# Optimization experiments

Measured on AMD Instinct MI355X. Metric: run time of the kernel, lower is better.

The kernel has to match this reference:

```python
import jax, jax.numpy as jnp
import numpy as np

B, L, F = 256, 1800, 50
E, K, H, D = 4, 2, 32, 64
MAXH, HU = 900, 32


def setup_inputs() -> dict:
    key = jax.random.key(0)
    ks = jax.random.split(key, 24)
    s = 0.1
    nrm = lambda k, shape: jax.random.normal(k, shape, jnp.float32) * s
    return {
        "x": jax.random.normal(ks[0], (B, L, F), jnp.float32),
        "horizon": jax.random.randint(ks[1], (B,), 0, MAXH + 1),
        "W_in": nrm(ks[2], (D, F)), "b_in": nrm(ks[3], (D,)),
        "emb": nrm(ks[4], (MAXH + 1, D)),
        "W_gate": nrm(ks[5], (E, D)), "b_gate": nrm(ks[6], (E,)),
        "Wih0": nrm(ks[7], (E, 3 * H, D)), "Whh0": nrm(ks[8], (E, 3 * H, H)),
        "bih0": nrm(ks[9], (E, 3 * H)), "bhh0": nrm(ks[10], (E, 3 * H)),
        "Wih1": nrm(ks[11], (E, 3 * H, H)), "Whh1": nrm(ks[12], (E, 3 * H, H)),
        "bih1": nrm(ks[13], (E, 3 * H)), "bhh1": nrm(ks[14], (E, 3 * H)),
        "Wh1": nrm(ks[15], (E, HU, H)), "bh1": nrm(ks[16], (E, HU)),
        "Wh2": nrm(ks[17], (E, 1, HU)), "bh2": nrm(ks[18], (E, 1)),
    }


def _gru_layer(x_seq, Wih, Whh, bih, bhh):
    # x_seq: (L, B, Din). PyTorch GRU cell math (gate order r, z, n).
    xg = jnp.einsum('lbd,gd->lbg', x_seq, Wih) + bih  # (L, B, 3H)
    h0 = jnp.zeros((x_seq.shape[1], H), x_seq.dtype)

    def step(h, xgt):
        gh = h @ Whh.T + bhh
        r = jax.nn.sigmoid(xgt[:, :H] + gh[:, :H])
        z = jax.nn.sigmoid(xgt[:, H:2 * H] + gh[:, H:2 * H])
        n = jnp.tanh(xgt[:, 2 * H:] + r * gh[:, 2 * H:])
        h_new = (1.0 - z) * n + z * h
        return h_new, h_new

    h_last, hs = jax.lax.scan(step, h0, xg)
    return h_last, hs


def _expert(x_seq, Wih0, Whh0, bih0, bhh0, Wih1, Whh1, bih1, bhh1, Wh1, bh1, Wh2, bh2):
    _, hs0 = _gru_layer(x_seq, Wih0, Whh0, bih0, bhh0)      # layer 0: full sequence
    h1, _ = _gru_layer(hs0, Wih1, Whh1, bih1, bhh1)          # layer 1: final hidden (B, H)
    hid = jax.nn.relu(h1 @ Wh1.T + bh1)                      # head MLP (eval: dropout = id)
    return (hid @ Wh2.T + bh2)[:, 0]                         # (B,)


def reference(x, horizon, W_in, b_in, emb, W_gate, b_gate,
              Wih0, Whh0, bih0, bhh0, Wih1, Whh1, bih1, bhh1,
              Wh1, bh1, Wh2, bh2):
    x_proj = jnp.einsum('blf,df->bld', x, W_in) + b_in       # input_proj
    h_embed = emb[horizon]                                   # (B, D)
    x_proj = x_proj + h_embed[:, None, :]
    gate_logits = h_embed @ W_gate.T + b_gate                # (B, E)
    topk_logits, topk_idx = jax.lax.top_k(gate_logits, K)
    topk_w = jax.nn.softmax(topk_logits, axis=-1)
    Bn = x.shape[0]
    # dense routing weights (B, E): zero for non-routed experts -> identical math
    w_dense = jnp.zeros((Bn, E), x.dtype).at[jnp.arange(Bn)[:, None], topk_idx].add(topk_w)
    x_seq = jnp.transpose(x_proj, (1, 0, 2))                 # (L, B, D)
    preds = jax.vmap(_expert, in_axes=(None,) + (0,) * 12)(
        x_seq, Wih0, Whh0, bih0, bhh0, Wih1, Whh1, bih1, bhh1, Wh1, bh1, Wh2, bh2)  # (E, B)
    return jnp.sum(w_dense.T * preds, axis=0)                # (B,)
```

## Files before the change

kernel.cpp:

```cpp
#include <hip/hip_runtime.h>
#include <math.h>

#define NB   256
#define LSEQ 1800
#define NF   50
#define NE   4
#define NH   32
#define G3   96
#define ND   64
#define NHU  32
#define CHUNK 72
#define TBLK  8
#define NCHUNK (LSEQ / CHUNK)
#define NBLK   (CHUNK / TBLK)

typedef float v2f __attribute__((ext_vector_type(2)));

__device__ __forceinline__ v2f v2fma(v2f a, v2f b, v2f c) {
    return __builtin_elementwise_fma(a, b, c);
}
__device__ __forceinline__ v2f mkv2(float a, float b) { v2f t; t.x = a; t.y = b; return t; }
__device__ __forceinline__ v2f splat2(float s) { v2f t; t.x = s; t.y = s; return t; }

__global__ void compute_C_kernel(const float* __restrict__ Wih0,
                                 const float* __restrict__ W_in,
                                 float* __restrict__ Cg) {
    int e = blockIdx.x;
    for (int idx = threadIdx.x; idx < NF * G3; idx += blockDim.x) {
        int f = idx / G3;
        int g = idx - f * G3;
        const float* wr = Wih0 + ((size_t)e * G3 + g) * ND;
        float s = 0.f;
        #pragma unroll 8
        for (int d = 0; d < ND; d++) s += wr[d] * W_in[d * NF + f];
        Cg[(size_t)e * NF * G3 + idx] = s;
    }
}

__device__ __forceinline__ float fsig(float x) {
    float e = __builtin_amdgcn_exp2f(-1.442695041f * x);
    return __builtin_amdgcn_rcpf(1.f + e);
}
__device__ __forceinline__ float ftanh(float x) {
    x = fmaxf(x, -20.f);
    float e = __builtin_amdgcn_exp2f(-2.885390082f * x);
    return (1.f - e) * __builtin_amdgcn_rcpf(1.f + e);
}

__global__ __launch_bounds__(64, 1)
void moe_gru_kernel(const float* __restrict__ x,
                    const int*   __restrict__ horizon,
                    const float* __restrict__ emb,
                    const float* __restrict__ W_gate,
                    const float* __restrict__ b_gate,
                    const float* __restrict__ b_in,
                    const float* __restrict__ Wih0,
                    const float* __restrict__ Whh0,
                    const float* __restrict__ bih0,
                    const float* __restrict__ bhh0,
                    const float* __restrict__ Wih1,
                    const float* __restrict__ Whh1,
                    const float* __restrict__ bih1,
                    const float* __restrict__ bhh1,
                    const float* __restrict__ Wh1,
                    const float* __restrict__ bh1,
                    const float* __restrict__ Wh2,
                    const float* __restrict__ bh2,
                    const float* __restrict__ Cg,
                    float* __restrict__ out) {
    __shared__ __align__(16) float smem[4800 + 3600 + 64 + 64 + 32];
    float* CT  = smem;
    float* xs  = smem + 4800;
    float* heL = smem + 4800 + 3600;
    float* bbL = heL + 64;
    float* h1L = bbL + 64;

    const int bid = blockIdx.x;
    const int b   = bid >> 2;
    const int e   = bid & 3;
    const int tid = threadIdx.x;
    const int j   = tid & 31;
    const int hlf = tid >> 5;
    const int k0h = hlf << 4;

    {
        int hor = horizon[b];
        float he = emb[(size_t)hor * ND + tid];
        heL[tid] = he;
        bbL[tid] = he + b_in[tid];
    }

    float lg[NE];
    #pragma unroll
    for (int q = 0; q < NE; q++) {
        float s = b_gate[q];
        for (int d = 0; d < ND; d++) s += heL[d] * W_gate[q * ND + d];
        lg[q] = s;
    }
    int i1 = 0;
    #pragma unroll
    for (int q = 1; q < NE; q++) if (lg[q] > lg[i1]) i1 = q;
    int i2 = (i1 == 0) ? 1 : 0;
    #pragma unroll
    for (int q = 0; q < NE; q++) if (q != i1 && lg[q] > lg[i2]) i2 = q;
    if (e != i1 && e != i2) return;
    const float ex2 = expf(lg[i2] - lg[i1]);
    const float wgt = (e == i1) ? (1.f / (1.f + ex2)) : (ex2 / (1.f + ex2));

    for (int idx = tid; idx < NF * G3; idx += 64)
        CT[idx] = Cg[(size_t)e * NF * G3 + idx];

    v2f sA0[16], sA1[16], sA2[16];
    v2f wB0[8], wB1[8], wB2[8];
    {
        const float* baseA = (hlf ? Wih1 : Whh0) + (size_t)e * G3 * NH;
        const float* rA0 = baseA + (size_t)j * NH;
        const float* rA1 = baseA + (size_t)(j + 32) * NH;
        const float* rA2 = baseA + (size_t)(j + 64) * NH;
        #pragma unroll
        for (int q4 = 0; q4 < 8; q4++) {
            float4 qa = ((const float4*)rA0)[q4];
            sA0[2*q4] = mkv2(qa.x, qa.y); sA0[2*q4+1] = mkv2(qa.z, qa.w);
            float4 qb = ((const float4*)rA1)[q4];
            sA1[2*q4] = mkv2(qb.x, qb.y); sA1[2*q4+1] = mkv2(qb.z, qb.w);
            float4 qc = ((const float4*)rA2)[q4];
            sA2[2*q4] = mkv2(qc.x, qc.y); sA2[2*q4+1] = mkv2(qc.z, qc.w);
        }
        const float* baseB = Whh1 + (size_t)e * G3 * NH;
        const float* rB0 = baseB + (size_t)j * NH + k0h;
        const float* rB1 = baseB + (size_t)(j + 32) * NH + k0h;
        const float* rB2 = baseB + (size_t)(j + 64) * NH + k0h;
        #pragma unroll
        for (int q4 = 0; q4 < 4; q4++) {
            float4 qa = ((const float4*)rB0)[q4];
            wB0[2*q4] = mkv2(qa.x, qa.y); wB0[2*q4+1] = mkv2(qa.z, qa.w);
            float4 qb = ((const float4*)rB1)[q4];
            wB1[2*q4] = mkv2(qb.x, qb.y); wB1[2*q4+1] = mkv2(qb.z, qb.w);
            float4 qc = ((const float4*)rB2)[q4];
            wB2[2*q4] = mkv2(qc.x, qc.y); wB2[2*q4+1] = mkv2(qc.z, qc.w);
        }
    }
    const float selb0 = hlf ? bih1[e*G3 + j]      : bhh0[e*G3 + j];
    const float selb1 = hlf ? bih1[e*G3 + j + 32] : bhh0[e*G3 + j + 32];
    const float selb2 = hlf ? bih1[e*G3 + j + 64] : bhh0[e*G3 + j + 64];
    const float whb0  = hlf ? 0.f : bhh1[e*G3 + j];
    const float whb1  = hlf ? 0.f : bhh1[e*G3 + j + 32];
    const float whb2  = hlf ? 0.f : bhh1[e*G3 + j + 64];

    float dreg0, dreg1, dreg2;
    {
        float s0 = bih0[e*G3 + j], s1 = bih0[e*G3 + j + 32], s2 = bih0[e*G3 + j + 64];
        const float* w0 = Wih0 + ((size_t)e * G3 + j) * ND;
        const float* w1 = Wih0 + ((size_t)e * G3 + j + 32) * ND;
        const float* w2 = Wih0 + ((size_t)e * G3 + j + 64) * ND;
        for (int d = 0; d < ND; d++) {
            float bb = bbL[d];
            s0 += w0[d] * bb; s1 += w1[d] * bb; s2 += w2[d] * bb;
        }
        dreg0 = hlf ? 0.f : s0;
        dreg1 = hlf ? 0.f : s1;
        dreg2 = hlf ? 0.f : s2;
    }

    v2f h0v[16], h1v[8];
    #pragma unroll
    for (int k = 0; k < 16; k++) h0v[k] = splat2(0.f);
    #pragma unroll
    for (int k = 0; k < 8; k++)  h1v[k] = splat2(0.f);
    float hold = 0.f;
    float lmul = hlf ? 0.f : 1.f;
    if (tid < 32) h1L[tid] = 0.f;

    const float* xg = x + (size_t)b * LSEQ * NF;

    for (int ch = 0; ch < NCHUNK; ch++) {
        {
            const float4* xc4 = (const float4*)(xg + (size_t)ch * CHUNK * NF);
            for (int i4 = tid; i4 < (CHUNK * NF) / 4; i4 += 64) {
                float4 v = xc4[i4];
                int idx = i4 * 4;
                #pragma unroll
                for (int u = 0; u < 4; u++) {
                    int id = idx + u;
                    int it = (int)(((unsigned)id * 5243u) >> 18);
                    int f  = id - it * 50;
                    float val = (u == 0) ? v.x : (u == 1) ? v.y : (u == 2) ? v.z : v.w;
                    xs[f * CHUNK + it] = val;
                }
            }
        }

        for (int blk = 0; blk < NBLK; blk++) {
            const int ib0 = blk * TBLK;
            v2f a0[4], a1[4], a2[4];
            #pragma unroll
            for (int p = 0; p < 4; p++) {
                a0[p] = splat2(dreg0); a1[p] = splat2(dreg1); a2[p] = splat2(dreg2);
            }
            {
                const int fb = 25 * hlf;
                #pragma unroll 5
                for (int f = 0; f < 25; f++) {
                    const int fg = fb + f;
                    float c0 = CT[fg * G3 + j];
                    float c1 = CT[fg * G3 + j + 32];
                    float c2 = CT[fg * G3 + j + 64];
                    const float4* xp = (const float4*)(xs + fg * CHUNK + ib0);
                    float4 xa = xp[0], xb = xp[1];
                    v2f xv[4] = { mkv2(xa.x, xa.y), mkv2(xa.z, xa.w),
                                  mkv2(xb.x, xb.y), mkv2(xb.z, xb.w) };
                    v2f w0 = splat2(c0), w1 = splat2(c1), w2 = splat2(c2);
                    #pragma unroll
                    for (int p = 0; p < 4; p++) {
                        a0[p] = v2fma(w0, xv[p], a0[p]);
                        a1[p] = v2fma(w1, xv[p], a1[p]);
                        a2[p] = v2fma(w2, xv[p], a2[p]);
                    }
                }
            }
            #pragma unroll
            for (int p = 0; p < 4; p++) {
                a0[p].x += __shfl_xor(a0[p].x, 32, 64); a0[p].y += __shfl_xor(a0[p].y, 32, 64);
                a1[p].x += __shfl_xor(a1[p].x, 32, 64); a1[p].y += __shfl_xor(a1[p].y, 32, 64);
                a2[p].x += __shfl_xor(a2[p].x, 32, 64); a2[p].y += __shfl_xor(a2[p].y, 32, 64);
            }

            #pragma unroll
            for (int i = 0; i < TBLK; i++) {
                v2f dB0 = mkv2(whb0, 0.f), dB1 = mkv2(whb1, 0.f), dB2 = mkv2(whb2, 0.f);
                #pragma unroll
                for (int k = 0; k < 8; k++) {
                    dB0 = v2fma(wB0[k], h1v[k], dB0);
                    dB1 = v2fma(wB1[k], h1v[k], dB1);
                    dB2 = v2fma(wB2[k], h1v[k], dB2);
                }
                float B0 = dB0.x + dB0.y, B1 = dB1.x + dB1.y, B2 = dB2.x + dB2.y;
                float R0 = B0 + __shfl_xor(B0, 32, 64);
                float R1 = B1 + __shfl_xor(B1, 32, 64);
                float R2 = B2 + __shfl_xor(B2, 32, 64);
                v2f dA0 = mkv2(selb0, 0.f), dA1 = mkv2(selb1, 0.f), dA2 = mkv2(selb2, 0.f);
                #pragma unroll
                for (int k = 0; k < 16; k++) {
                    dA0 = v2fma(sA0[k], h0v[k], dA0);
                    dA1 = v2fma(sA1[k], h0v[k], dA1);
                    dA2 = v2fma(sA2[k], h0v[k], dA2);
                }
                float A0 = dA0.x + dA0.y, A1 = dA1.x + dA1.y, A2 = dA2.x + dA2.y;
                const float ac0 = a0[i >> 1][i & 1];
                const float ac1 = a1[i >> 1][i & 1];
                const float ac2 = a2[i >> 1][i & 1];
                float o0   = hlf ? R0 : ac0;
                float o1   = hlf ? R1 : ac1;
                float npre = hlf ? A2 : ac2;
                float gn   = hlf ? R2 : A2;
                float r = fsig(A0 + o0);
                float z = fsig(A1 + o1);
                float n = ftanh(npre + r * gn);
                float hnew = (n + z * (hold - n)) * lmul;
                hold = hnew;
                lmul = 1.f;
                if (hlf) h1L[j] = hnew;
                const float4* h1q = (const float4*)(h1L + k0h);
                float4 q0 = h1q[0], q1 = h1q[1], q2 = h1q[2], q3 = h1q[3];
                h1v[0] = mkv2(q0.x, q0.y); h1v[1] = mkv2(q0.z, q0.w);
                h1v[2] = mkv2(q1.x, q1.y); h1v[3] = mkv2(q1.z, q1.w);
                h1v[4] = mkv2(q2.x, q2.y); h1v[5] = mkv2(q2.z, q2.w);
                h1v[6] = mkv2(q3.x, q3.y); h1v[7] = mkv2(q3.z, q3.w);
                {
                    int hni = __float_as_int(hnew);
                    #pragma unroll
                    for (int k = 0; k < 16; k++) {
                        float e0 = __int_as_float(__builtin_amdgcn_readlane(hni, 2*k));
                        float e1 = __int_as_float(__builtin_amdgcn_readlane(hni, 2*k+1));
                        h0v[k] = mkv2(e0, e1);
                    }
                }
            }
        }
    }

    {
        v2f dA0 = mkv2(selb0, 0.f), dA1 = mkv2(selb1, 0.f), dA2 = mkv2(selb2, 0.f);
        #pragma unroll
        for (int k = 0; k < 16; k++) {
            dA0 = v2fma(sA0[k], h0v[k], dA0);
            dA1 = v2fma(sA1[k], h0v[k], dA1);
            dA2 = v2fma(sA2[k], h0v[k], dA2);
        }
        v2f dB0 = mkv2(whb0, 0.f), dB1 = mkv2(whb1, 0.f), dB2 = mkv2(whb2, 0.f);
        #pragma unroll
        for (int k = 0; k < 8; k++) {
            dB0 = v2fma(wB0[k], h1v[k], dB0);
            dB1 = v2fma(wB1[k], h1v[k], dB1);
            dB2 = v2fma(wB2[k], h1v[k], dB2);
        }
        float A0 = dA0.x + dA0.y, A1 = dA1.x + dA1.y, A2 = dA2.x + dA2.y;
        float B0 = dB0.x + dB0.y, B1 = dB1.x + dB1.y, B2 = dB2.x + dB2.y;
        float R0 = B0 + __shfl_xor(B0, 32, 64);
        float R1 = B1 + __shfl_xor(B1, 32, 64);
        float R2 = B2 + __shfl_xor(B2, 32, 64);
        float r = fsig(A0 + R0);
        float z = fsig(A1 + R1);
        float n = ftanh(A2 + r * R2);
        float hfin = n + z * (hold - n);
        if (hlf) h1L[j] = hfin;
    }

    if (tid < 32) {
        float s = bh1[e * NHU + tid];
        const float* wr = Wh1 + ((size_t)e * NHU + tid) * NH;
        #pragma unroll
        for (int d = 0; d < NH; d++) s += wr[d] * h1L[d];
        float hid = fmaxf(s, 0.f);
        float c = hid * Wh2[e * NHU + tid];
        #pragma unroll
        for (int off = 16; off > 0; off >>= 1) c += __shfl_down(c, off, 64);
        if (tid == 0) atomicAdd(out + b, wgt * (c + bh2[e]));
    }
}

extern "C" void kernel_launch(void* const* d_in, const int* in_sizes, int n_in,
                              void* d_out, int out_size, void* d_ws, size_t ws_size,
                              hipStream_t stream) {
    const float* x       = (const float*)d_in[0];
    const int*   horizon = (const int*)  d_in[1];
    const float* W_in    = (const float*)d_in[2];
    const float* b_in    = (const float*)d_in[3];
    const float* emb     = (const float*)d_in[4];
    const float* W_gate  = (const float*)d_in[5];
    const float* b_gate  = (const float*)d_in[6];
    const float* Wih0    = (const float*)d_in[7];
    const float* Whh0    = (const float*)d_in[8];
    const float* bih0    = (const float*)d_in[9];
    const float* bhh0    = (const float*)d_in[10];
    const float* Wih1    = (const float*)d_in[11];
    const float* Whh1    = (const float*)d_in[12];
    const float* bih1    = (const float*)d_in[13];
    const float* bhh1    = (const float*)d_in[14];
    const float* Wh1     = (const float*)d_in[15];
    const float* bh1     = (const float*)d_in[16];
    const float* Wh2     = (const float*)d_in[17];
    const float* bh2     = (const float*)d_in[18];
    float* out = (float*)d_out;
    float* Cg  = (float*)d_ws;

    hipMemsetAsync(d_out, 0, NB * sizeof(float), stream);
    compute_C_kernel<<<dim3(NE), dim3(256), 0, stream>>>(Wih0, W_in, Cg);
    moe_gru_kernel<<<dim3(NB * NE), dim3(64), 0, stream>>>(
        x, horizon, emb, W_gate, b_gate, b_in,
        Wih0, Whh0, bih0, bhh0, Wih1, Whh1, bih1, bhh1,
        Wh1, bh1, Wh2, bh2, Cg, out);
}
```

Measured before the change: 1.333 ms.

## Pack eight routed batch rows per 512-thread block with compacted expert lists

```diff
diff --git a/kernel.cpp b/kernel.cpp
--- a/kernel.cpp
+++ b/kernel.cpp
@@ -9,10 +9,11 @@
 #define G3   96
 #define ND   64
 #define NHU  32
-#define CHUNK 72
+#define CHUNK 24
 #define TBLK  8
 #define NCHUNK (LSEQ / CHUNK)
 #define NBLK   (CHUNK / TBLK)
+#define WPB    8
 
 typedef float v2f __attribute__((ext_vector_type(2)));
 
@@ -47,7 +48,7 @@
     return (1.f - e) * __builtin_amdgcn_rcpf(1.f + e);
 }
 
-__global__ __launch_bounds__(64, 1)
+__global__ __launch_bounds__(512, 2)
 void moe_gru_kernel(const float* __restrict__ x,
                     const int*   __restrict__ horizon,
                     const float* __restrict__ emb,
@@ -68,47 +69,65 @@
                     const float* __restrict__ bh2,
                     const float* __restrict__ Cg,
                     float* __restrict__ out) {
-    __shared__ __align__(16) float smem[4800 + 3600 + 64 + 64 + 32];
+    __shared__ __align__(16) float smem[15688];
     float* CT  = smem;
-    float* xs  = smem + 4800;
-    float* heL = smem + 4800 + 3600;
-    float* bbL = heL + 64;
-    float* h1L = bbL + 64;
-
-    const int bid = blockIdx.x;
-    const int b   = bid >> 2;
-    const int e   = bid & 3;
-    const int tid = threadIdx.x;
-    const int j   = tid & 31;
-    const int hlf = tid >> 5;
-    const int k0h = hlf << 4;
+    float* wE  = smem + 15168;
+    int*   lst = (int*)(smem + 15424);
+    int*   pcnt = (int*)(smem + 15680);
+
+    const int e    = blockIdx.x;
+    const int t512 = threadIdx.x;
+    const int wave = t512 >> 6;
+    const int tid  = t512 & 63;
+    const int j    = tid & 31;
+    const int hlf  = tid >> 5;
+    const int k0h  = hlf << 4;
+
+    float* xs  = smem + 4800  + wave * (CHUNK * NF);
+    float* bbL = smem + 14400 + wave * 64;
+    float* h1L = smem + 14912 + wave * 32;
+
+    for (int idx = t512; idx < NF * G3; idx += 512)
+        CT[idx] = Cg[(size_t)e * NF * G3 + idx];
+    if (t512 < NB) {
+        int hor = horizon[t512];
+        const float* he = emb + (size_t)hor * ND;
+        float lg[NE];
+        #pragma unroll
+        for (int q = 0; q < NE; q++) {
+            float s = b_gate[q];
+            for (int d = 0; d < ND; d++) s += he[d] * W_gate[q * ND + d];
+            lg[q] = s;
+        }
+        int i1 = 0;
+        #pragma unroll
+        for (int q = 1; q < NE; q++) if (lg[q] > lg[i1]) i1 = q;
+        int i2 = (i1 == 0) ? 1 : 0;
+        #pragma unroll
+        for (int q = 0; q < NE; q++) if (q != i1 && lg[q] > lg[i2]) i2 = q;
+        float ex2 = expf(lg[i2] - lg[i1]);
+        float w1 = 1.f / (1.f + ex2);
+        float w2 = ex2 / (1.f + ex2);
+        wE[t512] = (e == i1) ? w1 : (e == i2) ? w2 : 0.f;
+    }
+    __syncthreads();
+    if (t512 == 0) {
+        int c = 0;
+        for (int t = 0; t < NB; t++) if (wE[t] > 0.f) lst[c++] = t;
+        *pcnt = c;
+    }
+    __syncthreads();
+
+    const int slot = blockIdx.y * WPB + wave;
+    const int cnt  = *pcnt;
+    if (slot >= cnt) return;
+    const int   b   = lst[slot];
+    const float wgt = wE[b];
 
     {
         int hor = horizon[b];
-        float he = emb[(size_t)hor * ND + tid];
-        heL[tid] = he;
-        bbL[tid] = he + b_in[tid];
-    }
-
-    float lg[NE];
-    #pragma unroll
-    for (int q = 0; q < NE; q++) {
-        float s = b_gate[q];
-        for (int d = 0; d < ND; d++) s += heL[d] * W_gate[q * ND + d];
-        lg[q] = s;
-    }
-    int i1 = 0;
-    #pragma unroll
-    for (int q = 1; q < NE; q++) if (lg[q] > lg[i1]) i1 = q;
-    int i2 = (i1 == 0) ? 1 : 0;
-    #pragma unroll
-    for (int q = 0; q < NE; q++) if (q != i1 && lg[q] > lg[i2]) i2 = q;
-    if (e != i1 && e != i2) return;
-    const float ex2 = expf(lg[i2] - lg[i1]);
-    const float wgt = (e == i1) ? (1.f / (1.f + ex2)) : (ex2 / (1.f + ex2));
-
-    for (int idx = tid; idx < NF * G3; idx += 64)
-        CT[idx] = Cg[(size_t)e * NF * G3 + idx];
+        bbL[tid] = emb[(size_t)hor * ND + tid] + b_in[tid];
+    }
 
     v2f sA0[16], sA1[16], sA2[16];
     v2f wB0[8], wB1[8], wB2[8];
@@ -346,7 +365,7 @@
 
     hipMemsetAsync(d_out, 0, NB * sizeof(float), stream);
     compute_C_kernel<<<dim3(NE), dim3(256), 0, stream>>>(Wih0, W_in, Cg);
-    moe_gru_kernel<<<dim3(NB * NE), dim3(64), 0, stream>>>(
+    moe_gru_kernel<<<dim3(NE, (NB + WPB - 1) / WPB), dim3(512), 0, stream>>>(
         x, horizon, emb, W_gate, b_gate, b_in,
         Wih0, Whh0, bih0, bhh0, Wih1, Whh1, bih1, bhh1,
         Wh1, bh1, Wh2, bh2, Cg, out);
```

New measurement: 1.876 ms. +40.7%, slower.

## Precompute routing lists and process two sequences per wavefront for ILP

Applied to the files above, without the earlier changes.

```diff
diff --git a/kernel.cpp b/kernel.cpp
--- a/kernel.cpp
+++ b/kernel.cpp
@@ -37,6 +37,42 @@
     }
 }
 
+__global__ void routing_kernel(const int*   __restrict__ horizon,
+                               const float* __restrict__ emb,
+                               const float* __restrict__ W_gate,
+                               const float* __restrict__ b_gate,
+                               int* __restrict__ lst, float* __restrict__ wl,
+                               int* __restrict__ cnt) {
+    __shared__ int scnt[NE];
+    const int t = threadIdx.x;
+    if (t < NE) scnt[t] = 0;
+    __syncthreads();
+    int hor = horizon[t];
+    const float* he = emb + (size_t)hor * ND;
+    float lg[NE];
+    #pragma unroll
+    for (int q = 0; q < NE; q++) {
+        float s = b_gate[q];
+        for (int d = 0; d < ND; d++) s += he[d] * W_gate[q * ND + d];
+        lg[q] = s;
+    }
+    int i1 = 0;
+    #pragma unroll
+    for (int q = 1; q < NE; q++) if (lg[q] > lg[i1]) i1 = q;
+    int i2 = (i1 == 0) ? 1 : 0;
+    #pragma unroll
+    for (int q = 0; q < NE; q++) if (q != i1 && lg[q] > lg[i2]) i2 = q;
+    float ex2 = expf(lg[i2] - lg[i1]);
+    float w1 = 1.f / (1.f + ex2);
+    float w2 = ex2 / (1.f + ex2);
+    int s1 = atomicAdd(&scnt[i1], 1);
+    lst[i1 * NB + s1] = t;  wl[i1 * NB + s1] = w1;
+    int s2 = atomicAdd(&scnt[i2], 1);
+    lst[i2 * NB + s2] = t;  wl[i2 * NB + s2] = w2;
+    __syncthreads();
+    if (t < NE) cnt[t] = scnt[t];
+}
+
 __device__ __forceinline__ float fsig(float x) {
     float e = __builtin_amdgcn_exp2f(-1.442695041f * x);
     return __builtin_amdgcn_rcpf(1.f + e);
@@ -51,8 +87,6 @@
 void moe_gru_kernel(const float* __restrict__ x,
                     const int*   __restrict__ horizon,
                     const float* __restrict__ emb,
-                    const float* __restrict__ W_gate,
-                    const float* __restrict__ b_gate,
                     const float* __restrict__ b_in,
                     const float* __restrict__ Wih0,
                     const float* __restrict__ Whh0,
@@ -67,48 +101,40 @@
                     const float* __restrict__ Wh2,
                     const float* __restrict__ bh2,
                     const float* __restrict__ Cg,
+                    const int*   __restrict__ lst,
+                    const float* __restrict__ wl,
+                    const int*   __restrict__ cnt,
                     float* __restrict__ out) {
-    __shared__ __align__(16) float smem[4800 + 3600 + 64 + 64 + 32];
+    __shared__ __align__(16) float smem[4800 + 2 * 3600 + 2 * 64 + 2 * 32];
     float* CT  = smem;
-    float* xs  = smem + 4800;
-    float* heL = smem + 4800 + 3600;
-    float* bbL = heL + 64;
-    float* h1L = bbL + 64;
-
-    const int bid = blockIdx.x;
-    const int b   = bid >> 2;
-    const int e   = bid & 3;
+    float* xsA = smem + 4800;
+    float* xsB = smem + 8400;
+    float* bbA = smem + 12000;
+    float* bbB = smem + 12064;
+    float* h1A = smem + 12128;
+    float* h1B = smem + 12160;
+
+    const int e   = blockIdx.x;
+    const int p   = blockIdx.y;
     const int tid = threadIdx.x;
     const int j   = tid & 31;
     const int hlf = tid >> 5;
     const int k0h = hlf << 4;
 
-    {
-        int hor = horizon[b];
-        float he = emb[(size_t)hor * ND + tid];
-        heL[tid] = he;
-        bbL[tid] = he + b_in[tid];
-    }
-
-    float lg[NE];
-    #pragma unroll
-    for (int q = 0; q < NE; q++) {
-        float s = b_gate[q];
-        for (int d = 0; d < ND; d++) s += heL[d] * W_gate[q * ND + d];
-        lg[q] = s;
-    }
-    int i1 = 0;
-    #pragma unroll
-    for (int q = 1; q < NE; q++) if (lg[q] > lg[i1]) i1 = q;
-    int i2 = (i1 == 0) ? 1 : 0;
-    #pragma unroll
-    for (int q = 0; q < NE; q++) if (q != i1 && lg[q] > lg[i2]) i2 = q;
-    if (e != i1 && e != i2) return;
-    const float ex2 = expf(lg[i2] - lg[i1]);
-    const float wgt = (e == i1) ? (1.f / (1.f + ex2)) : (ex2 / (1.f + ex2));
+    const int c  = cnt[e];
+    const int s0 = 2 * p;
+    if (s0 >= c) return;
+    const int   bA   = lst[e * NB + s0];
+    const float wgtA = wl[e * NB + s0];
+    const bool  hasB = (s0 + 1) < c;
+    const int   bB   = hasB ? lst[e * NB + s0 + 1] : bA;
+    const float wgtB = hasB ? wl[e * NB + s0 + 1] : 0.f;
 
     for (int idx = tid; idx < NF * G3; idx += 64)
         CT[idx] = Cg[(size_t)e * NF * G3 + idx];
+
+    bbA[tid] = emb[(size_t)horizon[bA] * ND + tid] + b_in[tid];
+    bbB[tid] = emb[(size_t)horizon[bB] * ND + tid] + b_in[tid];
 
     v2f sA0[16], sA1[16], sA2[16];
     v2f wB0[8], wB1[8], wB2[8];
@@ -147,55 +173,63 @@
     const float whb1  = hlf ? 0.f : bhh1[e*G3 + j + 32];
     const float whb2  = hlf ? 0.f : bhh1[e*G3 + j + 64];
 
-    float dreg0, dreg1, dreg2;
+    float dregA0, dregA1, dregA2, dregB0, dregB1, dregB2;
     {
-        float s0 = bih0[e*G3 + j], s1 = bih0[e*G3 + j + 32], s2 = bih0[e*G3 + j + 64];
         const float* w0 = Wih0 + ((size_t)e * G3 + j) * ND;
         const float* w1 = Wih0 + ((size_t)e * G3 + j + 32) * ND;
         const float* w2 = Wih0 + ((size_t)e * G3 + j + 64) * ND;
+        float a0 = bih0[e*G3 + j], a1 = bih0[e*G3 + j + 32], a2 = bih0[e*G3 + j + 64];
+        float b0 = a0, b1 = a1, b2 = a2;
         for (int d = 0; d < ND; d++) {
-            float bb = bbL[d];
-            s0 += w0[d] * bb; s1 += w1[d] * bb; s2 += w2[d] * bb;
-        }
-        dreg0 = hlf ? 0.f : s0;
-        dreg1 = hlf ? 0.f : s1;
-        dreg2 = hlf ? 0.f : s2;
-    }
-
-    v2f h0v[16], h1v[8];
+            float wv0 = w0[d], wv1 = w1[d], wv2 = w2[d];
+            float xa = bbA[d], xb = bbB[d];
+            a0 += wv0 * xa; a1 += wv1 * xa; a2 += wv2 * xa;
+            b0 += wv0 * xb; b1 += wv1 * xb; b2 += wv2 * xb;
+        }
+        dregA0 = hlf ? 0.f : a0; dregA1 = hlf ? 0.f : a1; dregA2 = hlf ? 0.f : a2;
+        dregB0 = hlf ? 0.f : b0; dregB1 = hlf ? 0.f : b1; dregB2 = hlf ? 0.f : b2;
+    }
+
+    v2f h0vA[16], h0vB[16], h1vA[8], h1vB[8];
     #pragma unroll
-    for (int k = 0; k < 16; k++) h0v[k] = splat2(0.f);
+    for (int k = 0; k < 16; k++) { h0vA[k] = splat2(0.f); h0vB[k] = splat2(0.f); }
     #pragma unroll
-    for (int k = 0; k < 8; k++)  h1v[k] = splat2(0.f);
-    float hold = 0.f;
+    for (int k = 0; k < 8; k++)  { h1vA[k] = splat2(0.f); h1vB[k] = splat2(0.f); }
+    float holdA = 0.f, holdB = 0.f;
     float lmul = hlf ? 0.f : 1.f;
-    if (tid < 32) h1L[tid] = 0.f;
-
-    const float* xg = x + (size_t)b * LSEQ * NF;
+    if (tid < 32) { h1A[tid] = 0.f; h1B[tid] = 0.f; }
+
+    const float* xgA = x + (size_t)bA * LSEQ * NF;
+    const float* xgB = x + (size_t)bB * LSEQ * NF;
 
     for (int ch = 0; ch < NCHUNK; ch++) {
         {
-            const float4* xc4 = (const float4*)(xg + (size_t)ch * CHUNK * NF);
+            const float4* xa4 = (const float4*)(xgA + (size_t)ch * CHUNK * NF);
+            const float4* xb4 = (const float4*)(xgB + (size_t)ch * CHUNK * NF);
             for (int i4 = tid; i4 < (CHUNK * NF) / 4; i4 += 64) {
-                float4 v = xc4[i4];
+                float4 va = xa4[i4];
+                float4 vb = xb4[i4];
                 int idx = i4 * 4;
                 #pragma unroll
                 for (int u = 0; u < 4; u++) {
                     int id = idx + u;
                     int it = (int)(((unsigned)id * 5243u) >> 18);
                     int f  = id - it * 50;
-                    float val = (u == 0) ? v.x : (u == 1) ? v.y : (u == 2) ? v.z : v.w;
-                    xs[f * CHUNK + it] = val;
+                    float fa = (u == 0) ? va.x : (u == 1) ? va.y : (u == 2) ? va.z : va.w;
+                    float fb = (u == 0) ? vb.x : (u == 1) ? vb.y : (u == 2) ? vb.z : vb.w;
+                    xsA[f * CHUNK + it] = fa;
+                    xsB[f * CHUNK + it] = fb;
                 }
             }
         }
 
         for (int blk = 0; blk < NBLK; blk++) {
             const int ib0 = blk * TBLK;
-            v2f a0[4], a1[4], a2[4];
+            v2f aA0[4], aA1[4], aA2[4], aB0[4], aB1[4], aB2[4];
             #pragma unroll
-            for (int p = 0; p < 4; p++) {
-                a0[p] = splat2(dreg0); a1[p] = splat2(dreg1); a2[p] = splat2(dreg2);
+            for (int q = 0; q < 4; q++) {
+                aA0[q] = splat2(dregA0); aA1[q] = splat2(dregA1); aA2[q] = splat2(dregA2);
+                aB0[q] = splat2(dregB0); aB1[q] = splat2(dregB1); aB2[q] = splat2(dregB2);
             }
             {
                 const int fb = 25 * hlf;
@@ -205,74 +239,116 @@
                     float c0 = CT[fg * G3 + j];
                     float c1 = CT[fg * G3 + j + 32];
                     float c2 = CT[fg * G3 + j + 64];
-                    const float4* xp = (const float4*)(xs + fg * CHUNK + ib0);
-                    float4 xa = xp[0], xb = xp[1];
-                    v2f xv[4] = { mkv2(xa.x, xa.y), mkv2(xa.z, xa.w),
-                                  mkv2(xb.x, xb.y), mkv2(xb.z, xb.w) };
+                    const float4* xpA = (const float4*)(xsA + fg * CHUNK + ib0);
+                    float4 xa = xpA[0], xb = xpA[1];
+                    v2f xvA[4] = { mkv2(xa.x, xa.y), mkv2(xa.z, xa.w),
+                                   mkv2(xb.x, xb.y), mkv2(xb.z, xb.w) };
+                    const float4* xpB = (const float4*)(xsB + fg * CHUNK + ib0);
+                    float4 ya = xpB[0], yb = xpB[1];
+                    v2f xvB[4] = { mkv2(ya.x, ya.y), mkv2(ya.z, ya.w),
+                                   mkv2(yb.x, yb.y), mkv2(yb.z, yb.w) };
                     v2f w0 = splat2(c0), w1 = splat2(c1), w2 = splat2(c2);
                     #pragma unroll
-                    for (int p = 0; p < 4; p++) {
-                        a0[p] = v2fma(w0, xv[p], a0[p]);
-                        a1[p] = v2fma(w1, xv[p], a1[p]);
-                        a2[p] = v2fma(w2, xv[p], a2[p]);
+                    for (int q = 0; q < 4; q++) {
+                        aA0[q] = v2fma(w0, xvA[q], aA0[q]);
+                        aA1[q] = v2fma(w1, xvA[q], aA1[q]);
+                        aA2[q] = v2fma(w2, xvA[q], aA2[q]);
+                        aB0[q] = v2fma(w0, xvB[q], aB0[q]);
+                        aB1[q] = v2fma(w1, xvB[q], aB1[q]);
+                        aB2[q] = v2fma(w2, xvB[q], aB2[q]);
                     }
                 }
             }
             #pragma unroll
-            for (int p = 0; p < 4; p++) {
-                a0[p].x += __shfl_xor(a0[p].x, 32, 64); a0[p].y += __shfl_xor(a0[p].y, 32, 64);
-                a1[p].x += __shfl_xor(a1[p].x, 32, 64); a1[p].y += __shfl_xor(a1[p].y, 32, 64);
-                a2[p].x += __shfl_xor(a2[p].x, 32, 64); a2[p].y += __shfl_xor(a2[p].y, 32, 64);
+            for (int q = 0; q < 4; q++) {
+                aA0[q].x += __shfl_xor(aA0[q].x, 32, 64); aA0[q].y += __shfl_xor(aA0[q].y, 32, 64);
+                aA1[q].x += __shfl_xor(aA1[q].x, 32, 64); aA1[q].y += __shfl_xor(aA1[q].y, 32, 64);
+                aA2[q].x += __shfl_xor(aA2[q].x, 32, 64); aA2[q].y += __shfl_xor(aA2[q].y, 32, 64);
+                aB0[q].x += __shfl_xor(aB0[q].x, 32, 64); aB0[q].y += __shfl_xor(aB0[q].y, 32, 64);
+                aB1[q].x += __shfl_xor(aB1[q].x, 32, 64); aB1[q].y += __shfl_xor(aB1[q].y, 32, 64);
+                aB2[q].x += __shfl_xor(aB2[q].x, 32, 64); aB2[q].y += __shfl_xor(aB2[q].y, 32, 64);
             }
 
             #pragma unroll
             for (int i = 0; i < TBLK; i++) {
-                v2f dB0 = mkv2(whb0, 0.f), dB1 = mkv2(whb1, 0.f), dB2 = mkv2(whb2, 0.f);
+                v2f dBA0 = mkv2(whb0, 0.f), dBA1 = mkv2(whb1, 0.f), dBA2 = mkv2(whb2, 0.f);
+                v2f dBB0 = mkv2(whb0, 0.f), dBB1 = mkv2(whb1, 0.f), dBB2 = mkv2(whb2, 0.f);
                 #pragma unroll
                 for (int k = 0; k < 8; k++) {
-                    dB0 = v2fma(wB0[k], h1v[k], dB0);
-                    dB1 = v2fma(wB1[k], h1v[k], dB1);
-                    dB2 = v2fma(wB2[k], h1v[k], dB2);
-                }
-                float B0 = dB0.x + dB0.y, B1 = dB1.x + dB1.y, B2 = dB2.x + dB2.y;
-                float R0 = B0 + __shfl_xor(B0, 32, 64);
-                float R1 = B1 + __shfl_xor(B1, 32, 64);
-                float R2 = B2 + __shfl_xor(B2, 32, 64);
-                v2f dA0 = mkv2(selb0, 0.f), dA1 = mkv2(selb1, 0.f), dA2 = mkv2(selb2, 0.f);
+                    dBA0 = v2fma(wB0[k], h1vA[k], dBA0);
+                    dBA1 = v2fma(wB1[k], h1vA[k], dBA1);
+                    dBA2 = v2fma(wB2[k], h1vA[k], dBA2);
+                    dBB0 = v2fma(wB0[k], h1vB[k], dBB0);
+                    dBB1 = v2fma(wB1[k], h1vB[k], dBB1);
+                    dBB2 = v2fma(wB2[k], h1vB[k], dBB2);
+                }
+                float BA0 = dBA0.x + dBA0.y, BA1 = dBA1.x + dBA1.y, BA2 = dBA2.x + dBA2.y;
+                float BB0 = dBB0.x + dBB0.y, BB1 = dBB1.x + dBB1.y, BB2 = dBB2.x + dBB2.y;
+                float RA0 = BA0 + __shfl_xor(BA0, 32, 64);
+                float RA1 = BA1 + __shfl_xor(BA1, 32, 64);
+                float RA2 = BA2 + __shfl_xor(BA2, 32, 64);
+                float RB0 = BB0 + __shfl_xor(BB0, 32, 64);
+                float RB1 = BB1 + __shfl_xor(BB1, 32, 64);
+                float RB2 = BB2 + __shfl_xor(BB2, 32, 64);
+                v2f dAA0 = mkv2(selb0, 0.f), dAA1 = mkv2(selb1, 0.f), dAA2 = mkv2(selb2, 0.f);
+                v2f dAB0 = mkv2(selb0, 0.f), dAB1 = mkv2(selb1, 0.f), dAB2 = mkv2(selb2, 0.f);
                 #pragma unroll
                 for (int k = 0; k < 16; k++) {
-                    dA0 = v2fma(sA0[k], h0v[k], dA0);
-                    dA1 = v2fma(sA1[k], h0v[k], dA1);
-                    dA2 = v2fma(sA2[k], h0v[k], dA2);
-                }
-                float A0 = dA0.x + dA0.y, A1 = dA1.x + dA1.y, A2 = dA2.x + dA2.y;
-                const float ac0 = a0[i >> 1][i & 1];
-                const float ac1 = a1[i >> 1][i & 1];
-                const float ac2 = a2[i >> 1][i & 1];
-                float o0   = hlf ? R0 : ac0;
-                float o1   = hlf ? R1 : ac1;
-                float npre = hlf ? A2 : ac2;
-                float gn   = hlf ? R2 : A2;
-                float r = fsig(A0 + o0);
-                float z = fsig(A1 + o1);
-                float n = ftanh(npre + r * gn);
-                float hnew = (n + z * (hold - n)) * lmul;
-                hold = hnew;
+                    dAA0 = v2fma(sA0[k], h0vA[k], dAA0);
+                    dAA1 = v2fma(sA1[k], h0vA[k], dAA1);
+                    dAA2 = v2fma(sA2[k], h0vA[k], dAA2);
+                    dAB0 = v2fma(sA0[k], h0vB[k], dAB0);
+                    dAB1 = v2fma(sA1[k], h0vB[k], dAB1);
+                    dAB2 = v2fma(sA2[k], h0vB[k], dAB2);
+                }
+                float AA0 = dAA0.x + dAA0.y, AA1 = dAA1.x + dAA1.y, AA2 = dAA2.x + dAA2.y;
+                float AB0 = dAB0.x + dAB0.y, AB1 = dAB1.x + dAB1.y, AB2 = dAB2.x + dAB2.y;
+                float acA0 = aA0[i >> 1][i & 1], acA1 = aA1[i >> 1][i & 1], acA2 = aA2[i >> 1][i & 1];
+                float acB0 = aB0[i >> 1][i & 1], acB1 = aB1[i >> 1][i & 1], acB2 = aB2[i >> 1][i & 1];
+                float oA0   = hlf ? RA0 : acA0;
+                float oA1   = hlf ? RA1 : acA1;
+                float npreA = hlf ? AA2 : acA2;
+                float gnA   = hlf ? RA2 : AA2;
+                float rA = fsig(AA0 + oA0);
+                float zA = fsig(AA1 + oA1);
+                float nA = ftanh(npreA + rA * gnA);
+                float hnewA = (nA + zA * (holdA - nA)) * lmul;
+                float oB0   = hlf ? RB0 : acB0;
+                float oB1   = hlf ? RB1 : acB1;
+                float npreB = hlf ? AB2 : acB2;
+                float gnB   = hlf ? RB2 : AB2;
+                float rB = fsig(AB0 + oB0);
+                float zB = fsig(AB1 + oB1);
+                float nB = ftanh(npreB + rB * gnB);
+                float hnewB = (nB + zB * (holdB - nB)) * lmul;
+                holdA = hnewA; holdB = hnewB;
                 lmul = 1.f;
-                if (hlf) h1L[j] = hnew;
-                const float4* h1q = (const float4*)(h1L + k0h);
-                float4 q0 = h1q[0], q1 = h1q[1], q2 = h1q[2], q3 = h1q[3];
-                h1v[0] = mkv2(q0.x, q0.y); h1v[1] = mkv2(q0.z, q0.w);
-                h1v[2] = mkv2(q1.x, q1.y); h1v[3] = mkv2(q1.z, q1.w);
-                h1v[4] = mkv2(q2.x, q2.y); h1v[5] = mkv2(q2.z, q2.w);
-                h1v[6] = mkv2(q3.x, q3.y); h1v[7] = mkv2(q3.z, q3.w);
+                if (hlf) { h1A[j] = hnewA; h1B[j] = hnewB; }
                 {
-                    int hni = __float_as_int(hnew);
+                    const float4* hqA = (const float4*)(h1A + k0h);
+                    float4 q0 = hqA[0], q1 = hqA[1], q2 = hqA[2], q3 = hqA[3];
+                    h1vA[0] = mkv2(q0.x, q0.y); h1vA[1] = mkv2(q0.z, q0.w);
+                    h1vA[2] = mkv2(q1.x, q1.y); h1vA[3] = mkv2(q1.z, q1.w);
+                    h1vA[4] = mkv2(q2.x, q2.y); h1vA[5] = mkv2(q2.z, q2.w);
+                    h1vA[6] = mkv2(q3.x, q3.y); h1vA[7] = mkv2(q3.z, q3.w);
+                    const float4* hqB = (const float4*)(h1B + k0h);
+                    float4 u0 = hqB[0], u1 = hqB[1], u2 = hqB[2], u3 = hqB[3];
+                    h1vB[0] = mkv2(u0.x, u0.y); h1vB[1] = mkv2(u0.z, u0.w);
+                    h1vB[2] = mkv2(u1.x, u1.y); h1vB[3] = mkv2(u1.z, u1.w);
+                    h1vB[4] = mkv2(u2.x, u2.y); h1vB[5] = mkv2(u2.z, u2.w);
+                    h1vB[6] = mkv2(u3.x, u3.y); h1vB[7] = mkv2(u3.z, u3.w);
+                }
+                {
+                    int hniA = __float_as_int(hnewA);
+                    int hniB = __float_as_int(hnewB);
                     #pragma unroll
                     for (int k = 0; k < 16; k++) {
-                        float e0 = __int_as_float(__builtin_amdgcn_readlane(hni, 2*k));
-                        float e1 = __int_as_float(__builtin_amdgcn_readlane(hni, 2*k+1));
-                        h0v[k] = mkv2(e0, e1);
+                        float a0e = __int_as_float(__builtin_amdgcn_readlane(hniA, 2*k));
+                        float a1e = __int_as_float(__builtin_amdgcn_readlane(hniA, 2*k+1));
+                        h0vA[k] = mkv2(a0e, a1e);
+                        float b0e = __int_as_float(__builtin_amdgcn_readlane(hniB, 2*k));
+                        float b1e = __int_as_float(__builtin_amdgcn_readlane(hniB, 2*k+1));
+                        h0vB[k] = mkv2(b0e, b1e);
                     }
                 }
             }
@@ -280,42 +356,64 @@
     }
 
     {
-        v2f dA0 = mkv2(selb0, 0.f), dA1 = mkv2(selb1, 0.f), dA2 = mkv2(selb2, 0.f);
+        v2f dAA0 = mkv2(selb0, 0.f), dAA1 = mkv2(selb1, 0.f), dAA2 = mkv2(selb2, 0.f);
+        v2f dAB0 = mkv2(selb0, 0.f), dAB1 = mkv2(selb1, 0.f), dAB2 = mkv2(selb2, 0.f);
         #pragma unroll
         for (int k = 0; k < 16; k++) {
-            dA0 = v2fma(sA0[k], h0v[k], dA0);
-            dA1 = v2fma(sA1[k], h0v[k], dA1);
-            dA2 = v2fma(sA2[k], h0v[k], dA2);
-        }
-        v2f dB0 = mkv2(whb0, 0.f), dB1 = mkv2(whb1, 0.f), dB2 = mkv2(whb2, 0.f);
+            dAA0 = v2fma(sA0[k], h0vA[k], dAA0);
+            dAA1 = v2fma(sA1[k], h0vA[k], dAA1);
+            dAA2 = v2fma(sA2[k], h0vA[k], dAA2);
+            dAB0 = v2fma(sA0[k], h0vB[k], dAB0);
+            dAB1 = v2fma(sA1[k], h0vB[k], dAB1);
+            dAB2 = v2fma(sA2[k], h0vB[k], dAB2);
+        }
+        v2f dBA0 = mkv2(whb0, 0.f), dBA1 = mkv2(whb1, 0.f), dBA2 = mkv2(whb2, 0.f);
+        v2f dBB0 = mkv2(whb0, 0.f), dBB1 = mkv2(whb1, 0.f), dBB2 = mkv2(whb2, 0.f);
         #pragma unroll
         for (int k = 0; k < 8; k++) {
-            dB0 = v2fma(wB0[k], h1v[k], dB0);
-            dB1 = v2fma(wB1[k], h1v[k], dB1);
-            dB2 = v2fma(wB2[k], h1v[k], dB2);
-        }
-        float A0 = dA0.x + dA0.y, A1 = dA1.x + dA1.y, A2 = dA2.x + dA2.y;
-        float B0 = dB0.x + dB0.y, B1 = dB1.x + dB1.y, B2 = dB2.x + dB2.y;
-        float R0 = B0 + __shfl_xor(B0, 32, 64);
-        float R1 = B1 + __shfl_xor(B1, 32, 64);
-        float R2 = B2 + __shfl_xor(B2, 32, 64);
-        float r = fsig(A0 + R0);
-        float z = fsig(A1 + R1);
-        float n = ftanh(A2 + r * R2);
-        float hfin = n + z * (hold - n);
-        if (hlf) h1L[j] = hfin;
-    }
-
-    if (tid < 32) {
-        float s = bh1[e * NHU + tid];
-        const float* wr = Wh1 + ((size_t)e * NHU + tid) * NH;
-        #pragma unroll
-        for (int d = 0; d < NH; d++) s += wr[d] * h1L[d];
+            dBA0 = v2fma(wB0[k], h1vA[k], dBA0);
+            dBA1 = v2fma(wB1[k], h1vA[k], dBA1);
+            dBA2 = v2fma(wB2[k], h1vA[k], dBA2);
+            dBB0 = v2fma(wB0[k], h1vB[k], dBB0);
+            dBB1 = v2fma(wB1[k], h1vB[k], dBB1);
+            dBB2 = v2fma(wB2[k], h1vB[k], dBB2);
+        }
+        float AA0 = dAA0.x + dAA0.y, AA1 = dAA1.x + dAA1.y, AA2 = dAA2.x + dAA2.y;
+        float AB0 = dAB0.x + dAB0.y, AB1 = dAB1.x + dAB1.y, AB2 = dAB2.x + dAB2.y;
+        float BA0 = dBA0.x + dBA0.y, BA1 = dBA1.x + dBA1.y, BA2 = dBA2.x + dBA2.y;
+        float BB0 = dBB0.x + dBB0.y, BB1 = dBB1.x + dBB1.y, BB2 = dBB2.x + dBB2.y;
+        float RA0 = BA0 + __shfl_xor(BA0, 32, 64);
+        float RA1 = BA1 + __shfl_xor(BA1, 32, 64);
+        float RA2 = BA2 + __shfl_xor(BA2, 32, 64);
+        float RB0 = BB0 + __shfl_xor(BB0, 32, 64);
+        float RB1 = BB1 + __shfl_xor(BB1, 32, 64);
+        float RB2 = BB2 + __shfl_xor(BB2, 32, 64);
+        float rA = fsig(AA0 + RA0);
+        float zA = fsig(AA1 + RA1);
+        float nA = ftanh(AA2 + rA * RA2);
+        float hfinA = nA + zA * (holdA - nA);
+        float rB = fsig(AB0 + RB0);
+        float zB = fsig(AB1 + RB1);
+        float nB = ftanh(AB2 + rB * RB2);
+        float hfinB = nB + zB * (holdB - nB);
+        if (hlf) { h1A[j] = hfinA; h1B[j] = hfinB; }
+    }
+
+    {
+        const float* hsrc = hlf ? h1B : h1A;
+        float s = bh1[e * NHU + j];
+        const float* wr = Wh1 + ((size_t)e * NHU + j) * NH;
+        #pragma unroll
+        for (int d = 0; d < NH; d++) s += wr[d] * hsrc[d];
         float hid = fmaxf(s, 0.f);
-        float c = hid * Wh2[e * NHU + tid];
-        #pragma unroll
-        for (int off = 16; off > 0; off >>= 1) c += __shfl_down(c, off, 64);
-        if (tid == 0) atomicAdd(out + b, wgt * (c + bh2[e]));
+        float cacc = hid * Wh2[e * NHU + j];
+        #pragma unroll
+        for (int off = 16; off > 0; off >>= 1) cacc += __shfl_down(cacc, off, 32);
+        if (j == 0) {
+            float w  = hlf ? wgtB : wgtA;
+            int   bo = hlf ? bB   : bA;
+            atomicAdd(out + bo, w * (cacc + bh2[e]));
+        }
     }
 }
 
@@ -342,12 +440,18 @@
     const float* Wh2     = (const float*)d_in[17];
     const float* bh2     = (const float*)d_in[18];
     float* out = (float*)d_out;
+
     float* Cg  = (float*)d_ws;
+    int*   lst = (int*)(Cg + NE * NF * G3);
+    float* wl  = (float*)(lst + NE * NB);
+    int*   cnt = (int*)(wl + NE * NB);
 
     hipMemsetAsync(d_out, 0, NB * sizeof(float), stream);
+    routing_kernel<<<dim3(1), dim3(NB), 0, stream>>>(horizon, emb, W_gate, b_gate,
+                                                     lst, wl, cnt);
     compute_C_kernel<<<dim3(NE), dim3(256), 0, stream>>>(Wih0, W_in, Cg);
-    moe_gru_kernel<<<dim3(NB * NE), dim3(64), 0, stream>>>(
-        x, horizon, emb, W_gate, b_gate, b_in,
+    moe_gru_kernel<<<dim3(NE, NB / 2), dim3(64), 0, stream>>>(
+        x, horizon, emb, b_in,
         Wih0, Whh0, bih0, bhh0, Wih1, Whh1, bih1, bhh1,
-        Wh1, bh1, Wh2, bh2, Cg, out);
-}
+        Wh1, bh1, Wh2, bh2, Cg, lst, wl, cnt, out);
+}
```

Measured after the change: 2.310 ms. +73.3%, slower.
